# Kernel optimization log

Hardware: AMD Instinct MI355X
Metric: run time of the kernel (lower is better)

## Reference

```python
import jax, jax.numpy as jnp
import numpy as np

B, L = 16, 54            # dialogues, utterances per dialogue
NDIM = 512; H = 512; NS = 2
T = B * L                # 864 utterances
N = 3 * T                # 2592 nodes (l,a,v per utterance)
NE = B * (L + 3)         # 912 hyperedges (3 modality + L utterance per dialogue)
NNZ = 6 * T              # 5184 incidence entries
E = B * 3 * L * (L - 1)  # 137376 directed intra-modality edges
NUM_L = 3; NUM_K = 4
EPS = 1e-8


def _build_indices():
    rng = np.random.default_rng(0)
    spk = rng.integers(0, NS, size=(B, L))
    # qmask [L, B, NS] one-hot of speakers (matches torch argmax path)
    qmask = np.eye(NS, dtype=np.float32)[spk].transpose(1, 0, 2)
    ar = np.arange(L)
    i1, i2, ht = [], [], []
    for d in range(B):
        base = d * 3 * L
        nl = base + ar; na = nl + L; nv = nl + 2 * L
        # 3 modality hyperedges then L per-utterance (l,a,v) hyperedges
        i1 += [nl, na, nv, np.stack([nl, na, nv], 1).reshape(-1)]
        eb = d * (L + 3)
        i2 += [np.repeat(eb + np.arange(3), L), np.repeat(eb + 3 + ar, 3)]
        ht += [np.ones(L, np.int64), np.zeros(3, np.int64)]
    hyperedge_index = np.stack([np.concatenate(i1), np.concatenate(i2)]).astype(np.int64)
    hyperedge_type = np.concatenate(ht)
    # full permutation edges within each modality of each dialogue
    s0 = np.repeat(ar, L); d0 = np.tile(ar, L)
    m = s0 != d0; s0, d0 = s0[m], d0[m]
    src, dst, et = [], [], []
    for d in range(B):
        same = (spk[d][s0] == spk[d][d0]).astype(np.int64)
        for mm in range(3):
            off = d * 3 * L + mm * L
            src.append(s0 + off); dst.append(d0 + off); et.append(same)
    edge_index = np.stack([np.concatenate(src), np.concatenate(dst)]).astype(np.int64)
    edge_type = np.concatenate(et)
    return qmask, hyperedge_index, hyperedge_type, edge_index, edge_type


def setup_inputs() -> dict:
    key = jax.random.key(0)
    ks = jax.random.split(key, 16)
    qmask, hei, het, ei, et = _build_indices()
    n = lambda k, s: jax.random.normal(k, s, dtype=jnp.float32)
    inp = {
        'a': n(ks[0], (T, NDIM)), 'v': n(ks[1], (T, NDIM)), 'l': n(ks[2], (T, NDIM)),
        'qmask': jnp.asarray(qmask),
        'spk_emb': n(ks[3], (NS, NDIM)) * 0.05,
        'fc1_W': n(ks[4], (NDIM, H)) * 0.05, 'fc1_b': jnp.zeros((H,), jnp.float32),
        'he_weight': jnp.ones((NE,), jnp.float32),
        'ew_weight': jnp.ones((NNZ,), jnp.float32),
        'he_attr1': jax.random.uniform(ks[5], (H,), dtype=jnp.float32),
        'he_attr2': jax.random.uniform(ks[6], (H,), dtype=jnp.float32),
        'hc_W': n(ks[7], (NUM_L, H, H)) * 0.05, 'hc_b': jnp.zeros((NUM_L, H), jnp.float32),
        'm3_W0': n(ks[8], (NUM_K, H, H)) * 0.05,
        'm3_W1': n(ks[9], (NUM_K, H, H)) * 0.05,
        'm3_Wself': n(ks[10], (NUM_K, H, H)) * 0.05,
        'm3_b': jnp.zeros((NUM_K, H), jnp.float32),
        'hyperedge_index': jnp.asarray(hei), 'hyperedge_type': jnp.asarray(het),
        'edge_index': jnp.asarray(ei), 'edge_type': jnp.asarray(et),
    }
    return inp


def reference(a, v, l, qmask, spk_emb, fc1_W, fc1_b, he_weight, ew_weight,
              he_attr1, he_attr2, hc_W, hc_b, m3_W0, m3_W1, m3_Wself, m3_b,
              hyperedge_index, hyperedge_type, edge_index, edge_type):
    seg = jax.ops.segment_sum
    # speaker embedding added to text modality (equal dia_len -> simple transpose)
    qm = qmask.transpose(1, 0, 2).reshape(T, NS)
    l = l + spk_emb[jnp.argmax(qm, axis=-1)]
    # per-dialogue node order: [l_d ; a_d ; v_d]
    feats = jnp.concatenate([l.reshape(B, L, NDIM), a.reshape(B, L, NDIM),
                             v.reshape(B, L, NDIM)], axis=1).reshape(N, NDIM)
    x1 = feats @ fc1_W + fc1_b
    node_i, edge_i = hyperedge_index[0], hyperedge_index[1]
    tfl = hyperedge_type.astype(x1.dtype)[:, None]
    edge_attr = he_attr1[None, :] * tfl + he_attr2[None, :] * (1.0 - tfl)  # [NE,H]
    out = x1
    for ll in range(NUM_L):  # hypergraph conv: gather->edge agg->scatter->linear
        de = seg(ew_weight, edge_i, num_segments=NE)
        e = seg(ew_weight[:, None] * out[node_i], edge_i, num_segments=NE)
        e = e / (de + EPS)[:, None] + edge_attr
        c = he_weight[edge_i]
        dn = seg(c, node_i, num_segments=N)
        agg = seg(c[:, None] * e[edge_i], node_i, num_segments=N) / (dn + EPS)[:, None]
        out = jax.nn.relu(agg @ hc_W[ll] + hc_b[ll])
    src, dst = edge_index[0], edge_index[1]
    same_spk = (edge_type == 1)[:, None]
    deg = seg(jnp.ones_like(dst, dtype=x1.dtype), dst, num_segments=N)
    gnn_out = x1
    denoise = jnp.float32(0.0)
    for kk in range(NUM_K):  # 2-relation RGCN-style denoise layer
        h0 = gnn_out @ m3_W0[kk]
        h1 = gnn_out @ m3_W1[kk]
        msg = jnp.where(same_spk, h1[src], h0[src])
        agg = seg(msg, dst, num_segments=N) / (deg + EPS)[:, None]
        f = jax.nn.relu(agg + gnn_out @ m3_Wself[kk] + m3_b[kk])
        denoise = jnp.mean(f * f)
        gnn_out = gnn_out + f
    return out + gnn_out, denoise
```

## Files before the change

### kernel.cpp

```cpp
#include <hip/hip_runtime.h>

typedef unsigned short ushort_t;
typedef __attribute__((ext_vector_type(4))) float f32x4;
typedef __attribute__((ext_vector_type(8))) short s16x8;
typedef __attribute__((ext_vector_type(8))) unsigned short u16x8;

#define NNODE 2592
#define MATSZ (512*512)
#define INV53 (1.0f/(53.0f + 1e-8f))

__device__ __forceinline__ ushort_t f2b(float f){
  union {unsigned int i; float f;} x; x.f = f;
  unsigned int r = (x.i + 0x7fffu + ((x.i>>16)&1u))>>16;
  return (ushort_t)r;
}

__device__ __forceinline__ void gemm32(const ushort_t* As,
    const ushort_t* W, int col0, f32x4 acc[2][2])
{
  const int tid = threadIdx.x;
  const int wave = tid>>6, lane = tid&63;
  const int ml = lane&15, quad = lane>>4;
  #pragma unroll
  for (int mf=0;mf<2;mf++)
    #pragma unroll
    for (int nf=0;nf<2;nf++) acc[mf][nf] = (f32x4){0.f,0.f,0.f,0.f};

  const ushort_t* bw0 = W + (size_t)(col0 + wave*32 + ml)*512 + quad*8;
  const ushort_t* bw1 = bw0 + (size_t)16*512;
  const int rsw = ml&7;
  #pragma unroll
  for (int ks=0; ks<16; ks++){
    const int chunk = ks*4 + quad;
    const int abase = (chunk>>3)*64 + (((chunk&7) ^ rsw)<<3);
    s16x8 a0 = *(const s16x8*)&As[(size_t)ml*512 + abase];
    s16x8 a1 = *(const s16x8*)&As[(size_t)(16+ml)*512 + abase];
    s16x8 b0 = *(const s16x8*)(bw0 + ks*32);
    s16x8 b1 = *(const s16x8*)(bw1 + ks*32);
    acc[0][0] = __builtin_amdgcn_mfma_f32_16x16x32_bf16(a0,b0,acc[0][0],0,0,0);
    acc[0][1] = __builtin_amdgcn_mfma_f32_16x16x32_bf16(a0,b1,acc[0][1],0,0,0);
    acc[1][0] = __builtin_amdgcn_mfma_f32_16x16x32_bf16(a1,b0,acc[1][0],0,0,0);
    acc[1][1] = __builtin_amdgcn_mfma_f32_16x16x32_bf16(a1,b1,acc[1][1],0,0,0);
  }
}

__device__ __forceinline__ void stageA_flat(ushort_t* As, const float* src, int r0){
  const int tid = threadIdx.x;
  int row = tid>>3, seg = tid&7;
  const float* p = src + (size_t)(r0+row)*512 + seg*64;
  int rsw = row&7;
  ushort_t* dstA = &As[row*512 + seg*64];
  #pragma unroll
  for (int j=0;j<8;j++){
    f32x4 xa = *(const f32x4*)(p+j*8), xb = *(const f32x4*)(p+j*8+4);
    u16x8 v;
    #pragma unroll
    for (int jj=0;jj<4;jj++){ v[jj]=f2b(xa[jj]); v[4+jj]=f2b(xb[jj]); }
    *(u16x8*)&dstA[(j ^ rsw)<<3] = v;
  }
}

__device__ __forceinline__ void transpose_tile(float (*tile)[65],
    const float* src, const float* src2, ushort_t* dst, int bx, int by)
{
  const int tid = threadIdx.x;
  int r0 = bx*64, c0 = by*64;
  #pragma unroll
  for (int j=0;j<4;j++){
    int idx = j*256 + tid;
    int r = idx>>4, c4 = (idx&15)*4;
    size_t off = (size_t)(r0+r)*512 + c0 + c4;
    f32x4 v = *(const f32x4*)&src[off];
    if (src2){
      f32x4 v2 = *(const f32x4*)&src2[off];
      #pragma unroll
      for (int jj=0;jj<4;jj++) v[jj] -= INV53 * v2[jj];
    }
    #pragma unroll
    for (int jj=0;jj<4;jj++) tile[r][c4+jj] = v[jj];
  }
  __syncthreads();
  #pragma unroll
  for (int j=0;j<2;j++){
    int idx = j*256 + tid;
    int c = idx>>3, r8 = (idx&7)*8;
    u16x8 v;
    #pragma unroll
    for (int tt=0;tt<8;tt++) v[tt] = f2b(tile[r8+tt][c]);
    *(u16x8*)&dst[(size_t)(c0+c)*512 + r0 + r8] = v;
  }
}

__global__ __launch_bounds__(256) void prep0_kernel(
    const float* __restrict__ fc1,
    const float* __restrict__ A_in, const float* __restrict__ V_in,
    const float* __restrict__ L_in, const float* __restrict__ qmask,
    const float* __restrict__ spk,
    ushort_t* __restrict__ WT, float* __restrict__ FS,
    float* __restrict__ cnts, float* __restrict__ acc,
    unsigned int* __restrict__ counter)
{
  __shared__ float tile[64][65];
  __shared__ unsigned char spks[54];
  const int tid = threadIdx.x;
  if (blockIdx.x < 48){
    if (blockIdx.x==0 && tid==0){ *acc = 0.f; *counter = 0u; }
    const int d = blockIdx.x/3, m = blockIdx.x - d*3;
    if (tid < 54)
      spks[tid] = qmask[(tid*16+d)*2+1] > qmask[(tid*16+d)*2];
    __syncthreads();
    float cnt1 = 0.f;
    #pragma unroll
    for (int i=0;i<54;i++) cnt1 += (float)spks[i];
    float cnt0 = 54.f - cnt1;
    const int col = tid*2;
    const float* base = (m==0)?L_in:(m==1)?A_in:V_in;
    float a0x=0.f,a0y=0.f,a1x=0.f,a1y=0.f;
    float b0x=0.f,b0y=0.f,b1x=0.f,b1y=0.f;
    for (int i=0;i<27;i++){
      float2 xa = *(const float2*)&base[(size_t)(d*54+i)*512 + col];
      float2 xb = *(const float2*)&base[(size_t)(d*54+i+27)*512 + col];
      if (spks[i])    { a1x+=xa.x; a1y+=xa.y; } else { a0x+=xa.x; a0y+=xa.y; }
      if (spks[i+27]) { b1x+=xb.x; b1y+=xb.y; } else { b0x+=xb.x; b0y+=xb.y; }
    }
    float s0x=a0x+b0x, s0y=a0y+b0y, s1x=a1x+b1x, s1y=a1y+b1y;
    if (m==0){
      float2 e0 = *(const float2*)&spk[col];
      float2 e1 = *(const float2*)&spk[512+col];
      s0x += cnt0*e0.x; s0y += cnt0*e0.y;
      s1x += cnt1*e1.x; s1y += cnt1*e1.y;
    }
    float2 o0; o0.x=s0x; o0.y=s0y;
    float2 o1; o1.x=s1x; o1.y=s1y;
    *(float2*)&FS[(size_t)(d*6+m*2  )*512 + col] = o0;
    *(float2*)&FS[(size_t)(d*6+m*2+1)*512 + col] = o1;
    if (m==0 && tid==0){ cnts[d*2]=cnt0; cnts[d*2+1]=cnt1; }
    return;
  }
  const int t = blockIdx.x - 48;
  transpose_tile(tile, fc1, nullptr, WT, t>>3, t&7);
}

__global__ __launch_bounds__(256) void fc1_kernel(
    const float* __restrict__ A_in, const float* __restrict__ V_in,
    const float* __restrict__ L_in, const float* __restrict__ qmask,
    const float* __restrict__ spk, const ushort_t* __restrict__ WTc,
    ushort_t* __restrict__ WT,
    const float* __restrict__ m0, const float* __restrict__ m1,
    const float* __restrict__ ms,
    const float* __restrict__ fc1_b, float* __restrict__ X1,
    const float* __restrict__ FS, const float* __restrict__ cnts,
    float* __restrict__ Gs)
{
  __shared__ __align__(16) union {
    ushort_t As[32*512];
    float tile[64][65];
  } sm;
  const int b = blockIdx.x, tid = threadIdx.x;
  const int wave = tid>>6, lane = tid&63;
  const int ml = lane&15, quad = lane>>4;
  if (b >= 336){
    const int bb = b - 336;
    const int w = 4 + (bb>>6), t = bb&63;
    const float* src = (w<8)  ? m0 + (size_t)(w-4)*MATSZ
                     : (w<12) ? m1 + (size_t)(w-8)*MATSZ
                              : ms + (size_t)(w-12)*MATSZ;
    const float* src2 = (w>=12) ? m1 + (size_t)(w-12)*MATSZ : nullptr;
    transpose_tile(sm.tile, src, src2, WT + (size_t)w*MATSZ, t>>3, t&7);
    return;
  }
  if (b < 324){
    const int r0 = (b>>2)*32, col0 = (b&3)*128;
    {
      int row = tid>>3, seg = tid&7, gr = r0+row;
      int d = gr/162, rm = gr-d*162, m = rm/54, i = rm-m*54, t = d*54+i;
      const float* pa = ((m==0)?L_in:(m==1)?A_in:V_in) + (size_t)t*512 + seg*64;
      const float* pb = pa;
      bool hassp = (m==0);
      if (hassp){
        int sp = qmask[(i*16+d)*2+1] > qmask[(i*16+d)*2];
        pb = spk + sp*512 + seg*64;
      }
      int rsw = row&7;
      ushort_t* dstA = &sm.As[row*512 + seg*64];
      #pragma unroll
      for (int j=0;j<8;j++){
        f32x4 xa = *(const f32x4*)(pa+j*8), xb = *(const f32x4*)(pa+j*8+4);
        if (hassp){
          f32x4 ya = *(const f32x4*)(pb+j*8), yb = *(const f32x4*)(pb+j*8+4);
          #pragma unroll
          for (int jj=0;jj<4;jj++){ xa[jj]+=ya[jj]; xb[jj]+=yb[jj]; }
        }
        u16x8 v;
        #pragma unroll
        for (int jj=0;jj<4;jj++){ v[jj]=f2b(xa[jj]); v[4+jj]=f2b(xb[jj]); }
        *(u16x8*)&dstA[(j ^ rsw)<<3] = v;
      }
    }
    __syncthreads();
    f32x4 acc[2][2];
    gemm32(sm.As, WTc, col0, acc);
    #pragma unroll
    for (int nf=0;nf<2;nf++){
      int col = col0 + wave*32 + nf*16 + ml;
      float bv = fc1_b[col];
      #pragma unroll
      for (int mf=0;mf<2;mf++)
        #pragma unroll
        for (int r=0;r<4;r++){
          int gr = r0 + mf*16 + quad*4 + r;
          X1[(size_t)gr*512 + col] = acc[mf][nf][r] + bv;
        }
    }
  } else {
    const int bb = b-324;
    const int r0 = (bb>>2)*32, col0 = (bb&3)*128;
    stageA_flat(sm.As, FS, r0);
    __syncthreads();
    f32x4 acc[2][2];
    gemm32(sm.As, WTc, col0, acc);
    #pragma unroll
    for (int nf=0;nf<2;nf++){
      int col = col0 + wave*32 + nf*16 + ml;
      float bv = fc1_b[col];
      #pragma unroll
      for (int mf=0;mf<2;mf++)
        #pragma unroll
        for (int r=0;r<4;r++){
          int gr = r0 + mf*16 + quad*4 + r;
          float cw = cnts[(gr/6)*2 + (gr&1)];
          Gs[(size_t)gr*512 + col] = acc[mf][nf][r] + cw*bv;
        }
    }
  }
}

__global__ __launch_bounds__(256) void ka_kernel(int kk,
    const float* __restrict__ gin, const float* __restrict__ Gs,
    const ushort_t* __restrict__ WT, const float* __restrict__ m3_b,
    float* __restrict__ HS, float* __restrict__ Sp,
    const float* __restrict__ edge_src, const float* __restrict__ ew_w,
    const int* __restrict__ het, const float* __restrict__ attr1,
    const float* __restrict__ attr2, float* __restrict__ EB,
    const float* __restrict__ hcW, ushort_t* __restrict__ WTmut)
{
  __shared__ __align__(16) union {
    ushort_t As[32*512];
    float tile[64][65];
  } sm;
  const int b = blockIdx.x, tid = threadIdx.x;
  const int wave = tid>>6, lane = tid&63;
  const int ml = lane&15, quad = lane>>4;
  if (b >= 1260){
    const int bb = b - 1260;
    const int w = 1 + (bb>>6), t = bb&63;
    transpose_tile(sm.tile, hcW + (size_t)(w-1)*MATSZ, nullptr,
                   WTmut + (size_t)w*MATSZ, t>>3, t&7);
    return;
  }
  if (b < 324){
    const int r0 = (b>>2)*32, col0 = (b&3)*128;
    stageA_flat(sm.As, gin, r0);
    __syncthreads();
    f32x4 acc[2][2];
    gemm32(sm.As, WT + (size_t)(12+kk)*MATSZ, col0, acc);
    #pragma unroll
    for (int nf=0;nf<2;nf++){
      int col = col0 + wave*32 + nf*16 + ml;
      float bv = m3_b[kk*512 + col];
      #pragma unroll
      for (int mf=0;mf<2;mf++)
        #pragma unroll
        for (int r=0;r<4;r++){
          int gr = r0 + mf*16 + quad*4 + r;
          HS[(size_t)gr*512 + col] = acc[mf][nf][r] + bv;
        }
    }
  } else if (b < 348){
    const int bb = b-324;
    const int rt = bb>>3, c8 = bb&7;
    const int r0 = rt*32, col0 = (c8&3)*128;
    const ushort_t* W = WT + (size_t)((c8<4 ? 4 : 8)+kk)*MATSZ;
    const int cb = (c8<4) ? 0 : 512;
    stageA_flat(sm.As, Gs, r0);
    __syncthreads();
    f32x4 acc[2][2];
    gemm32(sm.As, W, col0, acc);
    #pragma unroll
    for (int nf=0;nf<2;nf++){
      int col = cb + col0 + wave*32 + nf*16 + ml;
      #pragma unroll
      for (int mf=0;mf<2;mf++)
        #pragma unroll
        for (int r=0;r<4;r++){
          int row = r0 + mf*16 + quad*4 + r;
          Sp[(size_t)row*1024 + col] = acc[mf][nf][r];
        }
    }
  } else {
    int e = b - 348;
    int d = e/57, r = e - d*57;
    int col = tid*2;
    float sx=0.f, sy=0.f, de=0.f;
    if (r < 3){
      int nnz0 = d*324 + r*54;
      const float* row = edge_src + ((size_t)(d*162 + r*54))*512 + col;
      float sxa=0.f, sya=0.f, dea=0.f;
      float sxb=0.f, syb=0.f, deb=0.f;
      for (int i=0;i<27;i++){
        float wa = ew_w[nnz0+i];
        float wb = ew_w[nnz0+i+27];
        float2 xa = *(const float2*)(row + (size_t)i*512);
        float2 xb = *(const float2*)(row + (size_t)(i+27)*512);
        sxa += wa*xa.x; sya += wa*xa.y; dea += wa;
        sxb += wb*xb.x; syb += wb*xb.y; deb += wb;
      }
      sx = sxa+sxb; sy = sya+syb; de = dea+deb;
    } else {
      int i = r-3;
      int nnz0 = d*324 + 162 + i*3;
      #pragma unroll
      for (int m=0;m<3;m++){
        float w = ew_w[nnz0+m];
        const float* row = edge_src + ((size_t)(d*162 + m*54 + i))*512 + col;
        float2 x = *(const float2*)row;
        sx += w*x.x; sy += w*x.y; de += w;
      }
    }
    float invde = 1.0f/(de + 1e-8f);
    const float* at = het[e] ? attr1 : attr2;
    float2 o;
    o.x = sx*invde + at[col];
    o.y = sy*invde + at[col+1];
    *(float2*)(EB + (size_t)e*512 + col) = o;
  }
}

template<bool LAST>
__global__ __launch_bounds__(256) void kb_kernel(int lk,
    const float* __restrict__ EB, const ushort_t* __restrict__ WT,
    const float* __restrict__ hc_b, float* __restrict__ dst,
    const float* __restrict__ gin, const float* __restrict__ HS,
    const float* __restrict__ Sp, const float* __restrict__ qmask,
    const float* __restrict__ he_w,
    float* __restrict__ Gout, float* __restrict__ GsOut,
    const float* __restrict__ OUThg, float* __restrict__ dout,
    float* __restrict__ accp, unsigned int* __restrict__ counter)
{
  __shared__ __align__(16) union {
    ushort_t As[32*512];
    struct { unsigned char spks[54]; float red[256]; } sf;
  } sm;
  const int b = blockIdx.x, tid = threadIdx.x;
  if (!LAST && b < 324){
    const int r0 = (b>>2)*32, col0 = (b&3)*128;
    {
      int row = tid>>3, seg = tid&7, gr = r0+row;
      int d = gr/162, rm = gr-d*162, m = rm/54, i = rm-m*54;
      int em = d*57+m, eu = d*57+3+i;
      float w1 = he_w[em], w2 = he_w[eu], inv = 1.0f/(w1+w2+1e-8f);
      float c1 = w1*inv, c2 = w2*inv;
      const float* pa = EB + (size_t)em*512 + seg*64;
      const float* pb = EB + (size_t)eu*512 + seg*64;
      int rsw = row&7;
      ushort_t* dstA = &sm.As[row*512 + seg*64];
      #pragma unroll
      for (int j=0;j<8;j++){
        f32x4 xa = *(const f32x4*)(pa+j*8), xb = *(const f32x4*)(pa+j*8+4);
        f32x4 ya = *(const f32x4*)(pb+j*8), yb = *(const f32x4*)(pb+j*8+4);
        u16x8 v;
        #pragma unroll
        for (int jj=0;jj<4;jj++){
          v[jj]   = f2b(c1*xa[jj] + c2*ya[jj]);
          v[4+jj] = f2b(c1*xb[jj] + c2*yb[jj]);
        }
        *(u16x8*)&dstA[(j ^ rsw)<<3] = v;
      }
    }
    __syncthreads();
    f32x4 acc[2][2];
    gemm32(sm.As, WT + (size_t)(1+lk)*MATSZ, col0, acc);
    const int wave = tid>>6, lane = tid&63;
    const int ml = lane&15, quad = lane>>4;
    #pragma unroll
    for (int nf=0;nf<2;nf++){
      int col = col0 + wave*32 + nf*16 + ml;
      float bv = hc_b[lk*512 + col];
      #pragma unroll
      for (int mf=0;mf<2;mf++)
        #pragma unroll
        for (int r=0;r<4;r++){
          int gr = r0 + mf*16 + quad*4 + r;
          dst[(size_t)gr*512 + col] = fmaxf(acc[mf][nf][r] + bv, 0.f);
        }
    }
  } else {
    const int sfid = LAST ? b : b-324;
    const int g = sfid>>1, d = g/3;
    const int col = (sfid&1)*256 + tid;
    if (tid < 54)
      sm.sf.spks[tid] = qmask[(tid*16+d)*2+1] > qmask[(tid*16+d)*2];
    __syncthreads();
    const float* r0p = Sp + (size_t)(g*2)*1024;
    const float* r1p = Sp + (size_t)(g*2+1)*1024;
    float S1_0 = r0p[512+col];
    float S1_1 = r1p[512+col];
    float S0_0 = r1p[col];
    float S0_1 = r0p[col];
    size_t base = (size_t)g*54*512 + col;
    float gs0a=0.f, gs1a=0.f, sqa=0.f;
    float gs0b=0.f, gs1b=0.f, sqb=0.f;
    for (int i=0;i<27;i++){
      size_t offa = base + (size_t)i*512;
      size_t offb = base + (size_t)(i+27)*512;
      int spa = sm.sf.spks[i];
      int spb = sm.sf.spks[i+27];
      float hsa = HS[offa], gia = gin[offa];
      float hsb = HS[offb], gib = gin[offb];
      float S1a = spa ? S1_1 : S1_0, S0a = spa ? S0_1 : S0_0;
      float S1b = spb ? S1_1 : S1_0, S0b = spb ? S0_1 : S0_0;
      float fa = fmaxf((S1a + S0a)*INV53 + hsa, 0.f);
      float fb = fmaxf((S1b + S0b)*INV53 + hsb, 0.f);
      float gna = gia + fa;
      float gnb = gib + fb;
      if (LAST){
        sqa += fa*fa; sqb += fb*fb;
        dout[offa] = OUThg[offa] + gna;
        dout[offb] = OUThg[offb] + gnb;
      } else {
        Gout[offa] = gna;
        Gout[offb] = gnb;
        if (spa) gs1a += gna; else gs0a += gna;
        if (spb) gs1b += gnb; else gs0b += gnb;
      }
    }
    if (!LAST){
      GsOut[(size_t)(g*2)*512 + col]   = gs0a + gs0b;
      GsOut[(size_t)(g*2+1)*512 + col] = gs1a + gs1b;
    } else {
      sm.sf.red[tid] = sqa + sqb;
      __syncthreads();
      #pragma unroll
      for (int s=128; s>0; s>>=1){
        if (tid < s) sm.sf.red[tid] += sm.sf.red[tid+s];
        __syncthreads();
      }
      if (tid == 0){
        atomicAdd(accp, sm.sf.red[0]);
        __threadfence();
        unsigned int old = atomicAdd(counter, 1u);
        if (old == 95u)
          dout[(size_t)NNODE*512] = atomicAdd(accp, 0.0f) * (1.0f/1327104.0f);
      }
    }
  }
}

extern "C" void kernel_launch(void* const* d_in, const int* in_sizes, int n_in,
                              void* d_out, int out_size, void* d_ws, size_t ws_size,
                              hipStream_t stream)
{
  const float* A_in   = (const float*)d_in[0];
  const float* V_in   = (const float*)d_in[1];
  const float* L_in   = (const float*)d_in[2];
  const float* qmask  = (const float*)d_in[3];
  const float* spk    = (const float*)d_in[4];
  const float* fc1_W  = (const float*)d_in[5];
  const float* fc1_b  = (const float*)d_in[6];
  const float* he_w   = (const float*)d_in[7];
  const float* ew_w   = (const float*)d_in[8];
  const float* attr1  = (const float*)d_in[9];
  const float* attr2  = (const float*)d_in[10];
  const float* hc_W   = (const float*)d_in[11];
  const float* hc_b   = (const float*)d_in[12];
  const float* m3_W0  = (const float*)d_in[13];
  const float* m3_W1  = (const float*)d_in[14];
  const float* m3_Ws  = (const float*)d_in[15];
  const float* m3_b   = (const float*)d_in[16];
  const int*   het    = (const int*)d_in[18];
  float* dout = (float*)d_out;

  char* ws = (char*)d_ws;
  ushort_t* WT = (ushort_t*)ws;
  float* X1 = (float*)(ws + (size_t)16*MATSZ*2);
  float* OA = X1 + (size_t)NNODE*512;
  float* OB = OA + (size_t)NNODE*512;
  float* OC = OB + (size_t)NNODE*512;
  float* GA = OC + (size_t)NNODE*512;
  float* GB = GA + (size_t)NNODE*512;
  float* HS = GB + (size_t)NNODE*512;
  float* EB = HS + (size_t)NNODE*512;
  float* Sp = EB + (size_t)912*512;
  float* Gs = Sp + 96*1024;
  float* FS = Gs + 96*512;
  float* cnts = FS + 96*512;
  float* acc = cnts + 32;
  unsigned int* counter = (unsigned int*)(acc + 1);

  prep0_kernel<<<112,256,0,stream>>>(fc1_W, A_in, V_in, L_in, qmask, spk,
                                     WT, FS, cnts, acc, counter);
  fc1_kernel<<<1104,256,0,stream>>>(A_in, V_in, L_in, qmask, spk, WT, WT,
                                    m3_W0, m3_W1, m3_Ws, fc1_b,
                                    X1, FS, cnts, Gs);

  ka_kernel<<<1452,256,0,stream>>>(0, X1, Gs, WT, m3_b, HS, Sp,
                                   X1, ew_w, het, attr1, attr2, EB, hc_W, WT);
  kb_kernel<false><<<420,256,0,stream>>>(0, EB, WT, hc_b, OA, X1, HS, Sp,
      qmask, he_w, GA, Gs, nullptr, nullptr, acc, counter);
  ka_kernel<<<1260,256,0,stream>>>(1, GA, Gs, WT, m3_b, HS, Sp,
                                   OA, ew_w, het, attr1, attr2, EB, hc_W, WT);
  kb_kernel<false><<<420,256,0,stream>>>(1, EB, WT, hc_b, OB, GA, HS, Sp,
      qmask, he_w, GB, Gs, nullptr, nullptr, acc, counter);
  ka_kernel<<<1260,256,0,stream>>>(2, GB, Gs, WT, m3_b, HS, Sp,
                                   OB, ew_w, het, attr1, attr2, EB, hc_W, WT);
  kb_kernel<false><<<420,256,0,stream>>>(2, EB, WT, hc_b, OC, GB, HS, Sp,
      qmask, he_w, GA, Gs, nullptr, nullptr, acc, counter);
  ka_kernel<<<348,256,0,stream>>>(3, GA, Gs, WT, m3_b, HS, Sp,
                                  X1, ew_w, het, attr1, attr2, EB, hc_W, WT);
  kb_kernel<true><<<96,256,0,stream>>>(3, EB, WT, hc_b, nullptr, GA, HS, Sp,
      qmask, he_w, nullptr, nullptr, OC, dout, acc, counter);

  (void)in_sizes; (void)n_in; (void)out_size; (void)ws_size;
}
```

Measured before the change: 253.1 us.

## Defer weight transposes into later kb kernels to overlap with compute

Before this change, the fc1 and first ka kernels converted and transposed every per-layer weight matrix to bf16 up front. Now those launches handle only the matrices needed right away (fewer blocks). The remaining hc and m3 weight slots are transposed by extra blocks appended to each kb launch, just ahead of the layer that uses them. This spreads the conversion work into kernels that otherwise have underfilled grids, shortening the critical-path prologue. The risk is the extra blocks in each kb launch, and correctness depends on the slot schedule matching when each weight is first read.

```diff
diff --git a/kernel.cpp b/kernel.cpp
--- a/kernel.cpp
+++ b/kernel.cpp
@@ -91,6 +91,14 @@
   }
 }
 
+__device__ __forceinline__ const float* slot_src(int w, const float* hcW,
+    const float* m0w, const float* m1w, const float* msw){
+  return (w<4)  ? hcW + (size_t)(w-1)*MATSZ
+       : (w<8)  ? m0w + (size_t)(w-4)*MATSZ
+       : (w<12) ? m1w + (size_t)(w-8)*MATSZ
+                : msw + (size_t)(w-12)*MATSZ;
+}
+
 __global__ __launch_bounds__(256) void prep0_kernel(
     const float* __restrict__ fc1,
     const float* __restrict__ A_in, const float* __restrict__ V_in,
@@ -161,10 +169,8 @@
   const int ml = lane&15, quad = lane>>4;
   if (b >= 336){
     const int bb = b - 336;
-    const int w = 4 + (bb>>6), t = bb&63;
-    const float* src = (w<8)  ? m0 + (size_t)(w-4)*MATSZ
-                     : (w<12) ? m1 + (size_t)(w-8)*MATSZ
-                              : ms + (size_t)(w-12)*MATSZ;
+    const int w = 4 + ((bb>>6)<<2), t = bb&63;
+    const float* src = slot_src(w, nullptr, m0, m1, ms);
     const float* src2 = (w>=12) ? m1 + (size_t)(w-12)*MATSZ : nullptr;
     transpose_tile(sm.tile, src, src2, WT + (size_t)w*MATSZ, t>>3, t&7);
     return;
@@ -345,13 +351,26 @@
     const float* __restrict__ he_w,
     float* __restrict__ Gout, float* __restrict__ GsOut,
     const float* __restrict__ OUThg, float* __restrict__ dout,
-    float* __restrict__ accp, unsigned int* __restrict__ counter)
+    float* __restrict__ accp, unsigned int* __restrict__ counter,
+    int4 tsl, const float* __restrict__ hcW, const float* __restrict__ m0w,
+    const float* __restrict__ m1w, const float* __restrict__ msw,
+    ushort_t* __restrict__ WTmut)
 {
   __shared__ __align__(16) union {
     ushort_t As[32*512];
+    float tile[64][65];
     struct { unsigned char spks[54]; float red[256]; } sf;
   } sm;
   const int b = blockIdx.x, tid = threadIdx.x;
+  if (!LAST && b >= 420){
+    const int bb = b - 420;
+    const int wi = bb>>6, t = bb&63;
+    const int w = (wi==0)?tsl.x:(wi==1)?tsl.y:(wi==2)?tsl.z:tsl.w;
+    const float* src = slot_src(w, hcW, m0w, m1w, msw);
+    const float* src2 = (w>=12) ? m1w + (size_t)(w-12)*MATSZ : nullptr;
+    transpose_tile(sm.tile, src, src2, WTmut + (size_t)w*MATSZ, t>>3, t&7);
+    return;
+  }
   if (!LAST && b < 324){
     const int r0 = (b>>2)*32, col0 = (b&3)*128;
     {
@@ -497,28 +516,37 @@
   float* acc = cnts + 32;
   unsigned int* counter = (unsigned int*)(acc + 1);
 
+  const int4 tsl_d2 = make_int4(2, 5, 9, 13);
+  const int4 tsl_d4 = make_int4(3, 6, 10, 14);
+  const int4 tsl_d6 = make_int4(7, 11, 15, 0);
+  const int4 tsl_nil = make_int4(0, 0, 0, 0);
+
   prep0_kernel<<<112,256,0,stream>>>(fc1_W, A_in, V_in, L_in, qmask, spk,
                                      WT, FS, cnts, acc, counter);
-  fc1_kernel<<<1104,256,0,stream>>>(A_in, V_in, L_in, qmask, spk, WT, WT,
-                                    m3_W0, m3_W1, m3_Ws, fc1_b,
-                                    X1, FS, cnts, Gs);
-
-  ka_kernel<<<1452,256,0,stream>>>(0, X1, Gs, WT, m3_b, HS, Sp,
+  fc1_kernel<<<528,256,0,stream>>>(A_in, V_in, L_in, qmask, spk, WT, WT,
+                                   m3_W0, m3_W1, m3_Ws, fc1_b,
+                                   X1, FS, cnts, Gs);
+
+  ka_kernel<<<1324,256,0,stream>>>(0, X1, Gs, WT, m3_b, HS, Sp,
                                    X1, ew_w, het, attr1, attr2, EB, hc_W, WT);
-  kb_kernel<false><<<420,256,0,stream>>>(0, EB, WT, hc_b, OA, X1, HS, Sp,
-      qmask, he_w, GA, Gs, nullptr, nullptr, acc, counter);
+  kb_kernel<false><<<676,256,0,stream>>>(0, EB, WT, hc_b, OA, X1, HS, Sp,
+      qmask, he_w, GA, Gs, nullptr, nullptr, acc, counter,
+      tsl_d2, hc_W, m3_W0, m3_W1, m3_Ws, WT);
   ka_kernel<<<1260,256,0,stream>>>(1, GA, Gs, WT, m3_b, HS, Sp,
                                    OA, ew_w, het, attr1, attr2, EB, hc_W, WT);
-  kb_kernel<false><<<420,256,0,stream>>>(1, EB, WT, hc_b, OB, GA, HS, Sp,
-      qmask, he_w, GB, Gs, nullptr, nullptr, acc, counter);
+  kb_kernel<false><<<676,256,0,stream>>>(1, EB, WT, hc_b, OB, GA, HS, Sp,
+      qmask, he_w, GB, Gs, nullptr, nullptr, acc, counter,
+      tsl_d4, hc_W, m3_W0, m3_W1, m3_Ws, WT);
   ka_kernel<<<1260,256,0,stream>>>(2, GB, Gs, WT, m3_b, HS, Sp,
                                    OB, ew_w, het, attr1, attr2, EB, hc_W, WT);
-  kb_kernel<false><<<420,256,0,stream>>>(2, EB, WT, hc_b, OC, GB, HS, Sp,
-      qmask, he_w, GA, Gs, nullptr, nullptr, acc, counter);
+  kb_kernel<false><<<612,256,0,stream>>>(2, EB, WT, hc_b, OC, GB, HS, Sp,
+      qmask, he_w, GA, Gs, nullptr, nullptr, acc, counter,
+      tsl_d6, hc_W, m3_W0, m3_W1, m3_Ws, WT);
   ka_kernel<<<348,256,0,stream>>>(3, GA, Gs, WT, m3_b, HS, Sp,
                                   X1, ew_w, het, attr1, attr2, EB, hc_W, WT);
   kb_kernel<true><<<96,256,0,stream>>>(3, EB, WT, hc_b, nullptr, GA, HS, Sp,
-      qmask, he_w, nullptr, nullptr, OC, dout, acc, counter);
+      qmask, he_w, nullptr, nullptr, OC, dout, acc, counter,
+      tsl_nil, nullptr, nullptr, nullptr, nullptr, nullptr);
 
   (void)in_sizes; (void)n_in; (void)out_size; (void)ws_size;
 }
```

Result: no change. 251.1 us (-0.8%).
